# Kernel optimization log

Measured on AMD Instinct MI355X. Metric: run time of the kernel, lower is better.

The kernel has to match this reference:

```python
import jax, jax.numpy as jnp
import numpy as np

N_NODES = 50000
N_EDGES = 1250000
D = 64
EPS = 1e-07


def setup_inputs() -> dict:
    key = jax.random.key(0)
    ks = jax.random.split(key, 10)
    return {
        "node_feats": jax.random.normal(ks[0], (N_NODES, D), jnp.float32),
        "emb0": jax.random.normal(ks[1], (8, D), jnp.float32),
        "emb1": jax.random.normal(ks[2], (4, D), jnp.float32),
        "W": jax.random.normal(ks[3], (D, D), jnp.float32) / np.sqrt(D),
        "b": jnp.zeros((D,), jnp.float32),
        "beta": jnp.ones((1,), jnp.float32),
        "scale": jnp.ones((1,), jnp.float32),
        "src": jax.random.randint(ks[4], (N_EDGES,), 0, N_NODES),
        "dst": jax.random.randint(ks[5], (N_EDGES,), 0, N_NODES),
        "edge_feat0": jax.random.randint(ks[6], (N_EDGES,), 0, 8),
        "edge_feat1": jax.random.randint(ks[7], (N_EDGES,), 0, 4),
    }


def reference(node_feats, emb0, emb1, W, b, beta, scale, src, dst, edge_feat0, edge_feat1):
    n = node_feats.shape[0]
    # edge embeddings summed over categorical feature types
    e = emb0[edge_feat0] + emb1[edge_feat1]              # [E, D]
    # u_add_e then relu + eps
    m = jnp.maximum(node_feats[src] + e, 0.0) + EPS      # [E, D]
    # edge softmax over edges sharing the same destination (per feature dim)
    logits = m * beta                                    # [E, D]
    mx = jax.ops.segment_max(logits, dst, num_segments=n)
    ex = jnp.exp(logits - mx[dst])
    denom = jax.ops.segment_sum(ex, dst, num_segments=n)
    a = ex / denom[dst]                                  # [E, D]
    # scatter-sum aggregation of m * a to destination nodes
    msg = jax.ops.segment_sum(m * a, dst, num_segments=n)  # [N, D]
    # MessageNorm: L2-normalize msg, rescale by ||node_feats|| * scale
    msg_unit = msg / jnp.maximum(
        jnp.linalg.norm(msg, axis=-1, keepdims=True), 1e-12)
    feats_norm = jnp.linalg.norm(node_feats, axis=-1, keepdims=True)
    msg = msg_unit * feats_norm * scale
    # residual + single-layer MLP
    feats = node_feats + msg
    return feats @ W + b
```

## Files before the change

kernel.cpp:

```cpp
#include <hip/hip_runtime.h>

#define NN 50000
#define NE 1250000
#define DD 64
#define KR 391
#define RSH 7
#define RCAP 4096
#define RCSH 12


__global__ __launch_bounds__(512) void k_part(
    const int4* __restrict__ src4, const int4* __restrict__ dst4,
    const int4* __restrict__ ef04, const int4* __restrict__ ef14,
    const float* __restrict__ W, float* __restrict__ Wt,
    int* __restrict__ rcur, unsigned* __restrict__ staging)
{
    __shared__ int hist[KR], rbase[KR], cur[KR];
    const int t  = threadIdx.x;
    const int gb = blockIdx.x;

    for (int i = t; i < KR; i += 512) { hist[i] = 0; cur[i] = 0; }
    if (gb == 0)
        for (int i = t; i < 4096; i += 512)
            Wt[(i & 63) * DD + (i >> 6)] = W[i];
    __syncthreads();

    unsigned pay[8];
    int rr[8];
#pragma unroll
    for (int u = 0; u < 8; ++u) rr[u] = -1;

#pragma unroll
    for (int g = 0; g < 2; ++g) {
        const int i4 = gb * 1024 + t + g * 512;
        if (i4 < NE / 4) {
            const int4 s  = src4[i4], d = dst4[i4];
            const int4 f0 = ef04[i4], f1 = ef14[i4];
            const int ds[4] = {d.x, d.y, d.z, d.w};
            const int ss[4] = {s.x, s.y, s.z, s.w};
            const int a0[4] = {f0.x, f0.y, f0.z, f0.w};
            const int a1[4] = {f1.x, f1.y, f1.z, f1.w};
#pragma unroll
            for (int u = 0; u < 4; ++u) {
                const int k = g * 4 + u;
                rr[k]  = ds[u] >> RSH;
                pay[k] = (unsigned)ss[u] | ((unsigned)(a1[u] * 8 + a0[u]) << 16)
                         | ((unsigned)(ds[u] & 127) << 21);
            }
        }
    }
#pragma unroll
    for (int u = 0; u < 8; ++u)
        if (rr[u] >= 0) atomicAdd(&hist[rr[u]], 1);
    __syncthreads();

    for (int i = t; i < KR; i += 512) {
        const int h = hist[i];
        if (h) rbase[i] = atomicAdd(&rcur[i], h);
    }
    __syncthreads();

#pragma unroll
    for (int u = 0; u < 8; ++u) {
        if (rr[u] >= 0) {
            const int r   = rr[u];
            const int pos = rbase[r] + atomicAdd(&cur[r], 1);
            if (pos < RCAP) staging[(r << RCSH) + pos] = pay[u];
        }
    }
}

__global__ __launch_bounds__(256, 4) void genconv_agg(
    const float* __restrict__ nf,
    const float* __restrict__ emb0, const float* __restrict__ emb1,
    const float* __restrict__ Wt,  const float* __restrict__ b,
    const float* __restrict__ beta_p, const float* __restrict__ scale_p,
    const unsigned* __restrict__ staging, const int* __restrict__ rcur,
    float* __restrict__ out)
{
    __shared__ float emb_s[32 * DD];
    __shared__ float feat_s[4][DD];
    __shared__ unsigned buck[32 * DD];
    __shared__ int ldeg[32];

    const int t    = threadIdx.x;
    const int w    = t >> 6;
    const int lane = t & 63;
    const int r    = blockIdx.x >> 2;
    const int q    = blockIdx.x & 3;
    const int base_node = (r << RSH) + (q << 5);

    if (t < 32) ldeg[t] = 0;
    for (int i = t; i < 32 * DD; i += 256) {
        const int rr = i >> 6, c = i & 63;
        emb_s[i] = emb0[(rr & 7) * DD + c] + emb1[(rr >> 3) * DD + c];
    }

    float4 wc[16];
#pragma unroll
    for (int k = 0; k < 16; ++k)
        wc[k] = *(const float4*)(Wt + lane * DD + 4 * k);

    const float bias  = b[lane];
    const float beta  = beta_p[0];
    const float scale = scale_p[0];
    __syncthreads();

    const int ne = min(rcur[r], RCAP);
    const unsigned* sg = staging + (r << RCSH);
    for (int i = t; i < ne; i += 256) {
        const unsigned p = sg[i];
        const int d = (p >> 21) & 127;
        if ((d >> 5) == q) {
            const int dl  = d & 31;
            const int pos = atomicAdd(&ldeg[dl], 1);
            if (pos < DD) buck[(dl << 6) + pos] = p & 0x1FFFFFu;
        }
    }
    __syncthreads();

    const int nl0 = w << 3;
    unsigned pl = buck[(nl0 << 6) + lane];
    int cn = min(ldeg[nl0], DD);
    int node = base_node + nl0;
    float f = (node < NN) ? nf[(size_t)node * DD + lane] : 0.0f;

    for (int i = 0; i < 8; ++i) {
        const int nl = nl0 + i;
        node = base_node + nl;

        unsigned pl_n = 0u;
        int cn_n = 0;
        float f_n = 0.0f;
        if (i < 7) {
            pl_n = buck[((nl + 1) << 6) + lane];
            cn_n = ldeg[nl + 1];
            if (node + 1 < NN)
                f_n = nf[(size_t)(node + 1) * DD + lane];
        }

        float num = 0.0f, den = 0.0f;
        for (int j = 0; j < cn; j += 16) {
            float a[16];
            unsigned qv[16];
#pragma unroll
            for (int u = 0; u < 16; ++u) {
                const unsigned qq =
                    (unsigned)__builtin_amdgcn_readlane((int)pl, (j + u) & 63);
                qv[u] = qq;
                const int s = min((int)(qq & 0xFFFFu), NN - 1);
                a[u] = nf[(size_t)s * DD + lane];
            }
#pragma unroll
            for (int u = 0; u < 16; ++u) {
                const float eb = emb_s[(((qv[u] >> 16) & 31) << 6) + lane];
                const float m  = fmaxf(a[u] + eb, 0.0f) + 1e-7f;
                float x = __expf(beta * m);
                x = (j + u < cn) ? x : 0.0f;
                den += x;
                num = fmaf(m, x, num);
            }
        }

        const float msg = (den > 0.0f) ? num / den : 0.0f;

        float ss = msg * msg;
        float fs = f * f;
#pragma unroll
        for (int m = 32; m >= 1; m >>= 1) {
            ss += __shfl_xor(ss, m, 64);
            fs += __shfl_xor(fs, m, 64);
        }

        const float feat =
            f + msg * (1.0f / fmaxf(sqrtf(ss), 1e-12f)) * sqrtf(fs) * scale;

        feat_s[w][lane] = feat;

        float acc = bias;
#pragma unroll
        for (int k = 0; k < 16; ++k) {
            const float4 fv = *(const float4*)&feat_s[w][4 * k];
            acc = fmaf(fv.x, wc[k].x, acc);
            acc = fmaf(fv.y, wc[k].y, acc);
            acc = fmaf(fv.z, wc[k].z, acc);
            acc = fmaf(fv.w, wc[k].w, acc);
        }
        if (node < NN)
            out[(size_t)node * DD + lane] = acc;

        pl = pl_n;
        cn = min(cn_n, DD);
        f  = f_n;
    }
}

extern "C" void kernel_launch(void* const* d_in, const int* in_sizes, int n_in,
                              void* d_out, int out_size, void* d_ws, size_t ws_size,
                              hipStream_t stream)
{
    const float* nf    = (const float*)d_in[0];
    const float* emb0  = (const float*)d_in[1];
    const float* emb1  = (const float*)d_in[2];
    const float* W     = (const float*)d_in[3];
    const float* b     = (const float*)d_in[4];
    const float* beta  = (const float*)d_in[5];
    const float* scale = (const float*)d_in[6];
    const int* src = (const int*)d_in[7];
    const int* dst = (const int*)d_in[8];
    const int* ef0 = (const int*)d_in[9];
    const int* ef1 = (const int*)d_in[10];

    int*      rcur    = (int*)d_ws;
    int*      cnt     = rcur + 512;
    float*    Wt      = (float*)(cnt + 50048);
    unsigned* staging = (unsigned*)(Wt + 4096);

    hipMemsetAsync(rcur, 0, 512 * sizeof(int), stream);

    k_part<<<(NE / 4 + 1023) / 1024, 512, 0, stream>>>(
        (const int4*)src, (const int4*)dst, (const int4*)ef0, (const int4*)ef1,
        W, Wt, rcur, staging);

    genconv_agg<<<KR * 4, 256, 0, stream>>>(
        nf, emb0, emb1, Wt, b, beta, scale, staging, rcur, (float*)d_out);
}
```

Before: 197.4 us.

## Coarsen edge partition to 1024-node super-buckets shared by 32 aggregation blocks

The destination partition drops from 391 buckets of 128 nodes to 49 super-buckets of 1024 nodes, each with a 32K-entry staging region. Each aggregation block now scans a whole super-bucket and keeps only the edges for its 32 nodes. The partition kernel also now handles 4 edges per thread instead of 8, with twice as many blocks. The aim is fewer global bucket counters and cheaper partitioning, at the cost of every aggregation block reading roughly eight times as many staging entries, plus more atomic contention on the 49 global counters.

```diff
diff --git a/kernel.cpp b/kernel.cpp
--- a/kernel.cpp
+++ b/kernel.cpp
@@ -3,10 +3,10 @@
 #define NN 50000
 #define NE 1250000
 #define DD 64
-#define KR 391
-#define RSH 7
-#define RCAP 4096
-#define RCSH 12
+#define NSUP 49
+#define SSH 10
+#define SCAP 32768
+#define SCSH 15
 
 
 __global__ __launch_bounds__(512) void k_part(
@@ -15,57 +15,53 @@
     const float* __restrict__ W, float* __restrict__ Wt,
     int* __restrict__ rcur, unsigned* __restrict__ staging)
 {
-    __shared__ int hist[KR], rbase[KR], cur[KR];
+    __shared__ int hist[NSUP], rbase[NSUP], cur[NSUP];
     const int t  = threadIdx.x;
     const int gb = blockIdx.x;
 
-    for (int i = t; i < KR; i += 512) { hist[i] = 0; cur[i] = 0; }
+    if (t < NSUP) { hist[t] = 0; cur[t] = 0; }
     if (gb == 0)
         for (int i = t; i < 4096; i += 512)
             Wt[(i & 63) * DD + (i >> 6)] = W[i];
     __syncthreads();
 
-    unsigned pay[8];
-    int rr[8];
-#pragma unroll
-    for (int u = 0; u < 8; ++u) rr[u] = -1;
-
-#pragma unroll
-    for (int g = 0; g < 2; ++g) {
-        const int i4 = gb * 1024 + t + g * 512;
-        if (i4 < NE / 4) {
-            const int4 s  = src4[i4], d = dst4[i4];
-            const int4 f0 = ef04[i4], f1 = ef14[i4];
-            const int ds[4] = {d.x, d.y, d.z, d.w};
-            const int ss[4] = {s.x, s.y, s.z, s.w};
-            const int a0[4] = {f0.x, f0.y, f0.z, f0.w};
-            const int a1[4] = {f1.x, f1.y, f1.z, f1.w};
-#pragma unroll
-            for (int u = 0; u < 4; ++u) {
-                const int k = g * 4 + u;
-                rr[k]  = ds[u] >> RSH;
-                pay[k] = (unsigned)ss[u] | ((unsigned)(a1[u] * 8 + a0[u]) << 16)
-                         | ((unsigned)(ds[u] & 127) << 21);
-            }
-        }
-    }
-#pragma unroll
-    for (int u = 0; u < 8; ++u)
+    unsigned pay[4];
+    int rr[4];
+#pragma unroll
+    for (int u = 0; u < 4; ++u) rr[u] = -1;
+
+    const int i4 = gb * 512 + t;
+    if (i4 < NE / 4) {
+        const int4 s  = src4[i4], d = dst4[i4];
+        const int4 f0 = ef04[i4], f1 = ef14[i4];
+        const int ds[4] = {d.x, d.y, d.z, d.w};
+        const int ss[4] = {s.x, s.y, s.z, s.w};
+        const int a0[4] = {f0.x, f0.y, f0.z, f0.w};
+        const int a1[4] = {f1.x, f1.y, f1.z, f1.w};
+#pragma unroll
+        for (int u = 0; u < 4; ++u) {
+            rr[u]  = ds[u] >> SSH;
+            pay[u] = (unsigned)ss[u] | ((unsigned)(a1[u] * 8 + a0[u]) << 16)
+                     | ((unsigned)(ds[u] & 1023) << 21);
+        }
+    }
+#pragma unroll
+    for (int u = 0; u < 4; ++u)
         if (rr[u] >= 0) atomicAdd(&hist[rr[u]], 1);
     __syncthreads();
 
-    for (int i = t; i < KR; i += 512) {
-        const int h = hist[i];
-        if (h) rbase[i] = atomicAdd(&rcur[i], h);
-    }
-    __syncthreads();
-
-#pragma unroll
-    for (int u = 0; u < 8; ++u) {
+    if (t < NSUP) {
+        const int h = hist[t];
+        if (h) rbase[t] = atomicAdd(&rcur[t], h);
+    }
+    __syncthreads();
+
+#pragma unroll
+    for (int u = 0; u < 4; ++u) {
         if (rr[u] >= 0) {
             const int r   = rr[u];
             const int pos = rbase[r] + atomicAdd(&cur[r], 1);
-            if (pos < RCAP) staging[(r << RCSH) + pos] = pay[u];
+            if (pos < SCAP) staging[(r << SCSH) + pos] = pay[u];
         }
     }
 }
@@ -86,9 +82,9 @@
     const int t    = threadIdx.x;
     const int w    = t >> 6;
     const int lane = t & 63;
-    const int r    = blockIdx.x >> 2;
-    const int q    = blockIdx.x & 3;
-    const int base_node = (r << RSH) + (q << 5);
+    const int s    = blockIdx.x >> 5;
+    const int q    = blockIdx.x & 31;
+    const int base_node = (s << SSH) + (q << 5);
 
     if (t < 32) ldeg[t] = 0;
     for (int i = t; i < 32 * DD; i += 256) {
@@ -106,13 +102,12 @@
     const float scale = scale_p[0];
     __syncthreads();
 
-    const int ne = min(rcur[r], RCAP);
-    const unsigned* sg = staging + (r << RCSH);
+    const int ne = min(rcur[s], SCAP);
+    const unsigned* sg = staging + (s << SCSH);
     for (int i = t; i < ne; i += 256) {
         const unsigned p = sg[i];
-        const int d = (p >> 21) & 127;
-        if ((d >> 5) == q) {
-            const int dl  = d & 31;
+        if ((int)((p >> 26) & 31) == q) {
+            const int dl  = (p >> 21) & 31;
             const int pos = atomicAdd(&ldeg[dl], 1);
             if (pos < DD) buck[(dl << 6) + pos] = p & 0x1FFFFFu;
         }
@@ -148,8 +143,8 @@
                 const unsigned qq =
                     (unsigned)__builtin_amdgcn_readlane((int)pl, (j + u) & 63);
                 qv[u] = qq;
-                const int s = min((int)(qq & 0xFFFFu), NN - 1);
-                a[u] = nf[(size_t)s * DD + lane];
+                const int sidx = min((int)(qq & 0xFFFFu), NN - 1);
+                a[u] = nf[(size_t)sidx * DD + lane];
             }
 #pragma unroll
             for (int u = 0; u < 16; ++u) {
@@ -212,16 +207,15 @@
     const int* ef1 = (const int*)d_in[10];
 
     int*      rcur    = (int*)d_ws;
-    int*      cnt     = rcur + 512;
-    float*    Wt      = (float*)(cnt + 50048);
+    float*    Wt      = (float*)(rcur + 512);
     unsigned* staging = (unsigned*)(Wt + 4096);
 
     hipMemsetAsync(rcur, 0, 512 * sizeof(int), stream);
 
-    k_part<<<(NE / 4 + 1023) / 1024, 512, 0, stream>>>(
+    k_part<<<(NE / 4 + 511) / 512, 512, 0, stream>>>(
         (const int4*)src, (const int4*)dst, (const int4*)ef0, (const int4*)ef1,
         W, Wt, rcur, staging);
 
-    genconv_agg<<<KR * 4, 256, 0, stream>>>(
+    genconv_agg<<<NSUP * 32, 256, 0, stream>>>(
         nf, emb0, emb1, Wt, b, beta, scale, staging, rcur, (float*)d_out);
 }
```

New measurement: 254.0 us. 1.29x slower.
